# Performance work log

Measured on AMD Instinct MI355X. Metric: run time of the kernel, lower is better.

The kernel has to match this reference:

```python
import jax, jax.numpy as jnp
import numpy as np

B, C, N, D = 4, 128, 4096, 128  # batch, channels (=d_tran=out), points
BN_EPS = 1e-5


def setup_inputs() -> dict:
    key = jax.random.key(0)
    ks = jax.random.split(key, 10)
    s = 1.0 / np.sqrt(C)
    return {
        "x": jax.random.normal(ks[0], (B, C, N), dtype=jnp.float32),
        "Wqk": jax.random.uniform(ks[1], (D, C), minval=-s, maxval=s, dtype=jnp.float32),  # shared q/k weight
        "Wv": jax.random.uniform(ks[2], (D, C), minval=-s, maxval=s, dtype=jnp.float32),
        "bv": jax.random.uniform(ks[3], (D,), minval=-s, maxval=s, dtype=jnp.float32),
        "Wt": jax.random.uniform(ks[4], (C, D), minval=-s, maxval=s, dtype=jnp.float32),
        "bt": jax.random.uniform(ks[5], (C,), minval=-s, maxval=s, dtype=jnp.float32),
        "gamma": jnp.ones((C,), dtype=jnp.float32) + 0.1 * jax.random.normal(ks[6], (C,), dtype=jnp.float32),
        "beta": 0.1 * jax.random.normal(ks[7], (C,), dtype=jnp.float32),
        "rmean": 0.1 * jax.random.normal(ks[8], (C,), dtype=jnp.float32),
        "rvar": jax.random.uniform(ks[9], (C,), minval=0.5, maxval=1.5, dtype=jnp.float32),
    }


def reference(x, Wqk, Wv, bv, Wt, bt, gamma, beta, rmean, rvar):
    # x: [B, C, N]; 1x1 convs are per-point matmuls over the channel dim.
    x_q = jnp.einsum('dc,bcn->bnd', Wqk, x)                 # [B, N, D]
    x_k = jnp.einsum('dc,bcn->bdn', Wqk, x)                 # [B, D, N] (tied weight)
    x_v = jnp.einsum('dc,bcn->bdn', Wv, x) + bv[None, :, None]
    energy = jnp.einsum('bnd,bdm->bnm', x_q, x_k)           # [B, N, N]
    attention = jax.nn.softmax(energy, axis=-1)             # row softmax
    attention = attention / (1e-9 + attention.sum(axis=1, keepdims=True))  # L1 over columns
    x_r = jnp.einsum('bdn,bnm->bdm', x_v, attention)        # [B, D, N]
    y = jnp.einsum('od,bdn->bon', Wt, x - x_r) + bt[None, :, None]
    # BatchNorm1d, inference mode (running stats)
    y = gamma[None, :, None] * (y - rmean[None, :, None]) * jax.lax.rsqrt(rvar[None, :, None] + BN_EPS) + beta[None, :, None]
    return x + jax.nn.relu(y)
```

## Files before the change

kernel.cpp:

```cpp
#include <hip/hip_runtime.h>
#include <hip/hip_bf16.h>

typedef unsigned int u32;
typedef unsigned short u16;
using bf16x8 = __attribute__((ext_vector_type(8))) short;
using f32x4  = __attribute__((ext_vector_type(4))) float;
using f32x16 = __attribute__((ext_vector_type(16))) float;

#define B_ 4
#define C_ 128
#define N_ 4096
#define D_ 128
#define NS1 8
#define NSEG (N_ / NS1)
#define NCH (NSEG / 32)
#define NS2 6
#define NCHUNK (N_ / 32)

#define QS_STRIDE 136
#define VS_STRIDE 40
#define XS_STRIDE 68

__device__ __forceinline__ u16 f2bf(float f) {
    u32 x = __builtin_bit_cast(u32, f);
    x = x + 0x7fffu + ((x >> 16) & 1u);
    return (u16)(x >> 16);
}
__device__ __forceinline__ float bf2f(u16 h) {
    return __builtin_bit_cast(float, (u32)h << 16);
}
__device__ __forceinline__ u32 cvtpk(float lo, float hi) {
    u32 d;
    asm("v_cvt_pk_bf16_f32 %0, %1, %2" : "=v"(d) : "v"(lo), "v"(hi));
    return d;
}
#define EXP2 __builtin_amdgcn_exp2f
__device__ __forceinline__ bf16x8 pack8(const float* v, float s) {
    bf16x8 r;
#pragma unroll
    for (int j = 0; j < 8; ++j) r[j] = (short)f2bf(v[j] * s);
    return r;
}

__global__ __launch_bounds__(256) void k_proj(
        const float* __restrict__ x, const float* __restrict__ Wqk,
        const float* __restrict__ Wv, const float* __restrict__ bv,
        u16* __restrict__ Qbf, u16* __restrict__ Vbf) {
    __shared__ __align__(16) float xs[C_ * XS_STRIDE];
    const int bid = blockIdx.x;
    const int b  = bid >> 6;
    const int n0 = (bid & 63) << 6;
    const int t  = threadIdx.x;
    const float* xb = x + (size_t)b * C_ * N_;
#pragma unroll
    for (int i = 0; i < 8; ++i) {
        int idx = i * 256 + t;
        int c = idx >> 4, n4 = (idx & 15) * 4;
        *(float4*)&xs[c * XS_STRIDE + n4] = *(const float4*)&xb[(size_t)c * N_ + n0 + n4];
    }
    __syncthreads();
    const int lane = t & 63, w = t >> 6;
    const int l15 = lane & 15, g = lane >> 4;
    const float SC = 1.2011224087864498f;

    bf16x8 xf[4];
#pragma unroll
    for (int kk = 0; kk < 4; ++kk) {
        float tmp[8];
#pragma unroll
        for (int j = 0; j < 8; ++j) tmp[j] = xs[(kk * 32 + g * 8 + j) * XS_STRIDE + (16 * w + l15)];
        xf[kk] = pack8(tmp, 1.0f);
    }
    for (int dt = 0; dt < 8; ++dt) {
        const int d = dt * 16 + l15;
        bf16x8 wq[4], wv[4];
#pragma unroll
        for (int kk = 0; kk < 4; ++kk) {
            const float* pq = Wqk + (size_t)d * C_ + kk * 32 + g * 8;
            const float* pv = Wv  + (size_t)d * C_ + kk * 32 + g * 8;
            float a[8], c8[8];
#pragma unroll
            for (int j = 0; j < 8; ++j) { a[j] = pq[j]; c8[j] = pv[j]; }
            wq[kk] = pack8(a, SC);
            wv[kk] = pack8(c8, 1.0f);
        }
        f32x4 aq = {0.f, 0.f, 0.f, 0.f}, av = {0.f, 0.f, 0.f, 0.f};
        __builtin_amdgcn_s_setprio(1);
#pragma unroll
        for (int kk = 0; kk < 4; ++kk) {
            aq = __builtin_amdgcn_mfma_f32_16x16x32_bf16(xf[kk], wq[kk], aq, 0, 0, 0);
            av = __builtin_amdgcn_mfma_f32_16x16x32_bf16(wv[kk], xf[kk], av, 0, 0, 0);
        }
        __builtin_amdgcn_s_setprio(0);
#pragma unroll
        for (int r = 0; r < 4; ++r) {
            int nn = n0 + 16 * w + g * 4 + r;
            Qbf[((size_t)b * N_ + nn) * D_ + dt * 16 + l15] = f2bf(aq[r]);
            int dd = dt * 16 + g * 4 + r;
            Vbf[((size_t)b * D_ + dd) * N_ + n0 + 16 * w + l15] = f2bf(av[r] + bv[dd]);
        }
    }
}

__global__ __launch_bounds__(256, 4) void k_pass1(const u16* __restrict__ Qbf,
                                                  float* __restrict__ rsp) {
    __shared__ __align__(16) u16 qs[2][32 * QS_STRIDE];
    int bid = blockIdx.x;
    const int s = bid & 7; bid >>= 3;
    const int ntile = bid & 31; const int b = bid >> 5;
    const int t = threadIdx.x, lane = t & 63, w = t >> 6;
    const int l31 = lane & 31, hi = lane >> 5;
    const int nb = ntile * 128 + w * 32;

    bf16x8 bqn[8];
    {
        const u16* qn = Qbf + ((size_t)b * N_ + nb + l31) * D_ + hi * 8;
#pragma unroll
        for (int dblk = 0; dblk < 8; ++dblk) bqn[dblk] = *(const bf16x8*)(qn + dblk * 16);
    }
    const int srow = t >> 4, sslot = t & 15;
    const u16* qsrc = Qbf + ((size_t)b * N_ + s * NSEG + srow) * D_ + sslot * 8;
    const int qoff = srow * QS_STRIDE + sslot * 8;

    {
        uint4 a0 = *(const uint4*)qsrc;
        uint4 a1 = *(const uint4*)(qsrc + (size_t)16 * D_);
        *(uint4*)&qs[0][qoff] = a0;
        *(uint4*)&qs[0][qoff + 16 * QS_STRIDE] = a1;
    }
    __syncthreads();

    float rs0 = 0.f, rs1 = 0.f;
    for (int mc = 0; mc < NCH; ++mc) {
        const int cur = mc & 1;
        uint4 qpre0, qpre1;
        if (mc < NCH - 1) {
            qpre0 = *(const uint4*)(qsrc + (size_t)(mc + 1) * 32 * D_);
            qpre1 = *(const uint4*)(qsrc + (size_t)((mc + 1) * 32 + 16) * D_);
        }
        f32x16 ea, eb;
#pragma unroll
        for (int i = 0; i < 16; ++i) { ea[i] = 0.f; eb[i] = 0.f; }
        __builtin_amdgcn_s_setprio(1);
#pragma unroll
        for (int dblk = 0; dblk < 4; ++dblk) {
            bf16x8 am0 = *(const bf16x8*)(qs[cur] + l31 * QS_STRIDE + (2 * dblk + hi) * 8);
            bf16x8 am1 = *(const bf16x8*)(qs[cur] + l31 * QS_STRIDE + (2 * (dblk + 4) + hi) * 8);
            ea = __builtin_amdgcn_mfma_f32_32x32x16_bf16(am0, bqn[dblk], ea, 0, 0, 0);
            eb = __builtin_amdgcn_mfma_f32_32x32x16_bf16(am1, bqn[dblk + 4], eb, 0, 0, 0);
        }
        __builtin_amdgcn_s_setprio(0);
#pragma unroll
        for (int r = 0; r < 16; r += 2) {
            rs0 += EXP2(ea[r] + eb[r] - 64.0f);
            rs1 += EXP2(ea[r + 1] + eb[r + 1] - 64.0f);
        }
        if (mc < NCH - 1) {
            *(uint4*)&qs[cur ^ 1][qoff] = qpre0;
            *(uint4*)&qs[cur ^ 1][qoff + 16 * QS_STRIDE] = qpre1;
        }
        __syncthreads();
    }
    float rs = rs0 + rs1;
    rs += __shfl_xor(rs, 32);
    if (lane < 32) rsp[((size_t)s * B_ + b) * N_ + nb + l31] = rs;
}

__global__ void k_irs(const float* __restrict__ rsp, float* __restrict__ irs) {
    int i = blockIdx.x * 256 + threadIdx.x;
    if (i < B_ * N_) {
        float s = 0.f;
#pragma unroll
        for (int sp = 0; sp < NS1; ++sp) s += rsp[(size_t)sp * B_ * N_ + i];
        irs[i] = 1.0f / s;
    }
}

__global__ __launch_bounds__(256, 3) void k_pass2(
        const u16* __restrict__ Qbf, const u16* __restrict__ Vbf,
        const float* __restrict__ irs, u32* __restrict__ Rp32,
        float* __restrict__ csp) {
    __shared__ __align__(16) u16 qs[2][32 * QS_STRIDE];
    __shared__ __align__(16) u16 vs[2][128 * VS_STRIDE];
    int bid = blockIdx.x;
    const int s = bid % NS2; bid /= NS2;
    const int mtile = bid & 31; const int b = bid >> 5;
    const int t = threadIdx.x, lane = t & 63, w = t >> 6;
    const int l31 = lane & 31, hi = lane >> 5;
    const int m0 = mtile * 128 + w * 32;

    bf16x8 bq[8];
    {
        const u16* qm = Qbf + ((size_t)b * N_ + m0 + l31) * D_ + hi * 8;
#pragma unroll
        for (int dblk = 0; dblk < 8; ++dblk) bq[dblk] = *(const bf16x8*)(qm + dblk * 16);
    }
    f32x16 acc[4];
#pragma unroll
    for (int i = 0; i < 4; ++i)
#pragma unroll
        for (int r = 0; r < 16; ++r) acc[i][r] = 0.f;
    float cs = 0.f;
    const float* irsb = irs + (size_t)b * N_;

    const int qrow = t >> 4, qslot = t & 15;
    const u16* qsrc = Qbf + ((size_t)b * N_ + qrow) * D_ + qslot * 8;
    const int qoff = qrow * QS_STRIDE + qslot * 8;
    const int vd = t >> 2, vslot = t & 3;
    const u16* vsrc = Vbf + ((size_t)b * D_ + vd) * N_ + vslot * 8;
    const int voff = vd * VS_STRIDE + vslot * 8;

    {
        const u16* q0 = qsrc + (size_t)s * 32 * D_;
        const u16* v0 = vsrc + s * 32;
        uint4 a0 = *(const uint4*)q0;
        uint4 a1 = *(const uint4*)(q0 + (size_t)16 * D_);
        uint4 b0 = *(const uint4*)v0;
        uint4 b1 = *(const uint4*)(v0 + (size_t)64 * N_);
        *(uint4*)&qs[0][qoff] = a0;
        *(uint4*)&qs[0][qoff + 16 * QS_STRIDE] = a1;
        *(uint4*)&vs[0][voff] = b0;
        *(uint4*)&vs[0][voff + 64 * VS_STRIDE] = b1;
    }
    __syncthreads();

    int iter = 0;
    for (int c = s; c < NCHUNK; c += NS2, ++iter) {
        const int cur = iter & 1;
        const int nb = c * 32;
        const int cn = c + NS2;
        uint4 qpre0, qpre1, vpre0, vpre1;
        if (cn < NCHUNK) {
            const u16* qn = qsrc + (size_t)cn * 32 * D_;
            const u16* vn = vsrc + cn * 32;
            qpre0 = *(const uint4*)qn;
            qpre1 = *(const uint4*)(qn + (size_t)16 * D_);
            vpre0 = *(const uint4*)vn;
            vpre1 = *(const uint4*)(vn + (size_t)64 * N_);
        }
        const float* irp = irsb + nb;
        float si[32];
#pragma unroll
        for (int j = 0; j < 32; ++j) si[j] = irp[j];

        f32x16 ea, eb;
#pragma unroll
        for (int i = 0; i < 16; ++i) { ea[i] = 0.f; eb[i] = 0.f; }
        __builtin_amdgcn_s_setprio(1);
#pragma unroll
        for (int dblk = 0; dblk < 4; ++dblk) {
            bf16x8 aq0 = *(const bf16x8*)(qs[cur] + l31 * QS_STRIDE + (2 * dblk + hi) * 8);
            bf16x8 aq1 = *(const bf16x8*)(qs[cur] + l31 * QS_STRIDE + (2 * (dblk + 4) + hi) * 8);
            ea = __builtin_amdgcn_mfma_f32_32x32x16_bf16(aq0, bq[dblk], ea, 0, 0, 0);
            eb = __builtin_amdgcn_mfma_f32_32x32x16_bf16(aq1, bq[dblk + 4], eb, 0, 0, 0);
        }
        __builtin_amdgcn_s_setprio(0);
        uint4 bpA0, bpA1;
        {
            u32 A[8];
#pragma unroll
            for (int i = 0; i < 8; ++i) {
                const int cc = 2 * (i & 1) + 8 * (i >> 1);
                float ir0 = hi ? si[cc + 4] : si[cc];
                float ir1 = hi ? si[cc + 5] : si[cc + 1];
                float p0 = EXP2(ea[2 * i] + eb[2 * i] - 64.0f) * ir0;
                float p1 = EXP2(ea[2 * i + 1] + eb[2 * i + 1] - 64.0f) * ir1;
                cs += p0 + p1;
                A[i] = cvtpk(p0, p1);
            }
            u32 X0 = (u32)__shfl_xor((int)A[0], 32), X1 = (u32)__shfl_xor((int)A[1], 32);
            u32 X2 = (u32)__shfl_xor((int)A[2], 32), X3 = (u32)__shfl_xor((int)A[3], 32);
            u32 X4 = (u32)__shfl_xor((int)A[4], 32), X5 = (u32)__shfl_xor((int)A[5], 32);
            u32 X6 = (u32)__shfl_xor((int)A[6], 32), X7 = (u32)__shfl_xor((int)A[7], 32);
            bpA0 = (uint4){hi ? X2 : A[0], hi ? X3 : A[1], hi ? A[2] : X0, hi ? A[3] : X1};
            bpA1 = (uint4){hi ? X6 : A[4], hi ? X7 : A[5], hi ? A[6] : X4, hi ? A[7] : X5};
        }
        __builtin_amdgcn_s_setprio(1);
#pragma unroll
        for (int nblk = 0; nblk < 2; ++nblk) {
            bf16x8 bp = __builtin_bit_cast(bf16x8, nblk ? bpA1 : bpA0);
#pragma unroll
            for (int dblk = 0; dblk < 4; ++dblk) {
                bf16x8 av = *(const bf16x8*)(vs[cur] + (dblk * 32 + l31) * VS_STRIDE +
                                             (nblk * 2 + hi) * 8);
                acc[dblk] = __builtin_amdgcn_mfma_f32_32x32x16_bf16(av, bp, acc[dblk], 0, 0, 0);
            }
        }
        __builtin_amdgcn_s_setprio(0);
        if (cn < NCHUNK) {
            *(uint4*)&qs[cur ^ 1][qoff] = qpre0;
            *(uint4*)&qs[cur ^ 1][qoff + 16 * QS_STRIDE] = qpre1;
            *(uint4*)&vs[cur ^ 1][voff] = vpre0;
            *(uint4*)&vs[cur ^ 1][voff + 64 * VS_STRIDE] = vpre1;
        }
        __syncthreads();
    }
    cs += __shfl_xor(cs, 32);
    if (lane < 32) csp[((size_t)s * B_ + b) * N_ + m0 + l31] = cs;
    u32* rpb = Rp32 + ((size_t)s * B_ + b) * (size_t)(D_ / 2) * N_;
#pragma unroll
    for (int dblk = 0; dblk < 4; ++dblk) {
#pragma unroll
        for (int j = 0; j < 8; ++j) {
            const int row = dblk * 16 + (j & 1) + 4 * (j >> 1) + 2 * hi;
            u32 pk = cvtpk(acc[dblk][2 * j], acc[dblk][2 * j + 1]);
            rpb[(size_t)row * N_ + m0 + l31] = pk;
        }
    }
}

__global__ __launch_bounds__(512) void k_final(
        const float* __restrict__ x, const float* __restrict__ Wt,
        const float* __restrict__ bt, const float* __restrict__ gamma,
        const float* __restrict__ beta, const float* __restrict__ rmean,
        const float* __restrict__ rvar, const u32* __restrict__ Rp32,
        const float* __restrict__ csp, float* __restrict__ out) {
    __shared__ float us[128 * 65];
    __shared__ float icss[64];
    const int bid = blockIdx.x;
    const int b = bid >> 6;
    const int n0 = (bid & 63) << 6;
    const int t = threadIdx.x, lane = t & 63, w = t >> 6;
    const int l15 = lane & 15, g = lane >> 4;
    if (t < 64) {
        float s = 0.f;
#pragma unroll
        for (int sp = 0; sp < NS2; ++sp)
            s += csp[((size_t)sp * B_ + b) * N_ + n0 + t];
        icss[t] = 1.0f / (1e-9f + s);
    }
    __syncthreads();
    const float* xb = x + (size_t)b * C_ * N_;
    for (int i = 0; i < 8; ++i) {
        int idx = i * 512 + t;
        int dp = idx >> 6, n = idx & 63;
        float r0 = 0.f, r1 = 0.f;
#pragma unroll
        for (int sp = 0; sp < NS2; ++sp) {
            u32 v = Rp32[(((size_t)(sp * B_ + b) * (D_ / 2)) + dp) * N_ + n0 + n];
            r0 += bf2f((u16)(v & 0xffffu));
            r1 += bf2f((u16)(v >> 16));
        }
        float ic = icss[n];
        us[(2 * dp) * 65 + n]     = xb[(size_t)(2 * dp) * N_ + n0 + n]     - r0 * ic;
        us[(2 * dp + 1) * 65 + n] = xb[(size_t)(2 * dp + 1) * N_ + n0 + n] - r1 * ic;
    }
    __syncthreads();
    const int cg = w & 3;
    const int ct0 = (w >> 2) * 4;
    bf16x8 uf[4];
#pragma unroll
    for (int kk = 0; kk < 4; ++kk) {
        float tmp[8];
#pragma unroll
        for (int j = 0; j < 8; ++j) tmp[j] = us[(kk * 32 + g * 8 + j) * 65 + (16 * cg + l15)];
        uf[kk] = pack8(tmp, 1.0f);
    }
    for (int cti = 0; cti < 4; ++cti) {
        const int ct = ct0 + cti;
        const int c = ct * 16 + l15;
        bf16x8 wf[4];
#pragma unroll
        for (int kk = 0; kk < 4; ++kk) {
            const float* p = Wt + (size_t)c * D_ + kk * 32 + g * 8;
            float a[8];
#pragma unroll
            for (int j = 0; j < 8; ++j) a[j] = p[j];
            wf[kk] = pack8(a, 1.0f);
        }
        f32x4 acc = {0.f, 0.f, 0.f, 0.f};
        __builtin_amdgcn_s_setprio(1);
#pragma unroll
        for (int kk = 0; kk < 4; ++kk)
            acc = __builtin_amdgcn_mfma_f32_16x16x32_bf16(wf[kk], uf[kk], acc, 0, 0, 0);
        __builtin_amdgcn_s_setprio(0);
#pragma unroll
        for (int r = 0; r < 4; ++r) {
            const int cc = ct * 16 + g * 4 + r;
            const int nn = n0 + 16 * cg + l15;
            float y = acc[r] + bt[cc];
            float bn = gamma[cc] * (y - rmean[cc]) * rsqrtf(rvar[cc] + 1e-5f) + beta[cc];
            float rl = fmaxf(bn, 0.0f);
            out[((size_t)b * C_ + cc) * N_ + nn] = xb[(size_t)cc * N_ + nn] + rl;
        }
    }
}

extern "C" void kernel_launch(void* const* d_in, const int* in_sizes, int n_in,
                              void* d_out, int out_size, void* d_ws, size_t ws_size,
                              hipStream_t stream) {
    (void)in_sizes; (void)n_in; (void)out_size; (void)ws_size;
    const float* x     = (const float*)d_in[0];
    const float* Wqk   = (const float*)d_in[1];
    const float* Wv    = (const float*)d_in[2];
    const float* bv    = (const float*)d_in[3];
    const float* Wt    = (const float*)d_in[4];
    const float* bt    = (const float*)d_in[5];
    const float* gamma = (const float*)d_in[6];
    const float* beta  = (const float*)d_in[7];
    const float* rmean = (const float*)d_in[8];
    const float* rvar  = (const float*)d_in[9];
    float* out = (float*)d_out;

    char* ws = (char*)d_ws;
    u16*   Qbf = (u16*)(ws);
    u16*   Vbf = (u16*)(ws + 4194304);
    float* rsp = (float*)(ws + 8388608);
    float* irs = (float*)(ws + 8912896);
    float* csp = (float*)(ws + 8978432);
    u32*   Rp  = (u32*)(ws + 9371648);

    k_proj  <<<B_ * 64,       256, 0, stream>>>(x, Wqk, Wv, bv, Qbf, Vbf);
    k_pass1 <<<B_ * 32 * NS1, 256, 0, stream>>>(Qbf, rsp);
    k_irs   <<<(B_ * N_ + 255) / 256, 256, 0, stream>>>(rsp, irs);
    k_pass2 <<<B_ * 32 * NS2, 256, 0, stream>>>(Qbf, Vbf, irs, Rp, csp);
    k_final <<<B_ * 64,       512, 0, stream>>>(x, Wt, bt, gamma, beta, rmean, rvar, Rp, csp, out);
}
```

Baseline: 113.2 us.

## Enlarge pass1 row tile to 512 per block with 512 threads

The row-sum pass now uses 512-thread blocks. Each wave holds two 32-row Q fragments in registers, so each block covers 512 rows, and each staged key chunk in shared memory is reused across twice as many rows. To keep the grid size up, the key dimension is split into 16 segments instead of 8, which doubles the rsp partial buffer and moves the later workspace offsets. The aim is fewer global/LDS loads per MFMA, at the cost of higher register pressure and extra partial sums for k_irs to reduce.

```diff
diff --git a/kernel.cpp b/kernel.cpp
--- a/kernel.cpp
+++ b/kernel.cpp
@@ -11,7 +11,7 @@
 #define C_ 128
 #define N_ 4096
 #define D_ 128
-#define NS1 8
+#define NS1 16
 #define NSEG (N_ / NS1)
 #define NCH (NSEG / 32)
 #define NS2 6
@@ -102,21 +102,25 @@
     }
 }
 
-__global__ __launch_bounds__(256, 4) void k_pass1(const u16* __restrict__ Qbf,
+__global__ __launch_bounds__(512, 4) void k_pass1(const u16* __restrict__ Qbf,
                                                   float* __restrict__ rsp) {
     __shared__ __align__(16) u16 qs[2][32 * QS_STRIDE];
     int bid = blockIdx.x;
-    const int s = bid & 7; bid >>= 3;
-    const int ntile = bid & 31; const int b = bid >> 5;
+    const int s = bid % NS1; bid /= NS1;
+    const int ntile = bid & 7; const int b = bid >> 3;
     const int t = threadIdx.x, lane = t & 63, w = t >> 6;
     const int l31 = lane & 31, hi = lane >> 5;
-    const int nb = ntile * 128 + w * 32;
-
-    bf16x8 bqn[8];
+    const int nb0 = ntile * 512 + w * 64;
+
+    bf16x8 bqn0[8], bqn1[8];
     {
-        const u16* qn = Qbf + ((size_t)b * N_ + nb + l31) * D_ + hi * 8;
-#pragma unroll
-        for (int dblk = 0; dblk < 8; ++dblk) bqn[dblk] = *(const bf16x8*)(qn + dblk * 16);
+        const u16* qn0 = Qbf + ((size_t)b * N_ + nb0 + l31) * D_ + hi * 8;
+        const u16* qn1 = qn0 + (size_t)32 * D_;
+#pragma unroll
+        for (int dblk = 0; dblk < 8; ++dblk) {
+            bqn0[dblk] = *(const bf16x8*)(qn0 + dblk * 16);
+            bqn1[dblk] = *(const bf16x8*)(qn1 + dblk * 16);
+        }
     }
     const int srow = t >> 4, sslot = t & 15;
     const u16* qsrc = Qbf + ((size_t)b * N_ + s * NSEG + srow) * D_ + sslot * 8;
@@ -124,46 +128,63 @@
 
     {
         uint4 a0 = *(const uint4*)qsrc;
-        uint4 a1 = *(const uint4*)(qsrc + (size_t)16 * D_);
         *(uint4*)&qs[0][qoff] = a0;
-        *(uint4*)&qs[0][qoff + 16 * QS_STRIDE] = a1;
     }
     __syncthreads();
 
-    float rs0 = 0.f, rs1 = 0.f;
+    float rs0 = 0.f, rs1 = 0.f, rs2 = 0.f, rs3 = 0.f;
     for (int mc = 0; mc < NCH; ++mc) {
         const int cur = mc & 1;
-        uint4 qpre0, qpre1;
-        if (mc < NCH - 1) {
-            qpre0 = *(const uint4*)(qsrc + (size_t)(mc + 1) * 32 * D_);
-            qpre1 = *(const uint4*)(qsrc + (size_t)((mc + 1) * 32 + 16) * D_);
-        }
-        f32x16 ea, eb;
-#pragma unroll
-        for (int i = 0; i < 16; ++i) { ea[i] = 0.f; eb[i] = 0.f; }
-        __builtin_amdgcn_s_setprio(1);
-#pragma unroll
-        for (int dblk = 0; dblk < 4; ++dblk) {
-            bf16x8 am0 = *(const bf16x8*)(qs[cur] + l31 * QS_STRIDE + (2 * dblk + hi) * 8);
-            bf16x8 am1 = *(const bf16x8*)(qs[cur] + l31 * QS_STRIDE + (2 * (dblk + 4) + hi) * 8);
-            ea = __builtin_amdgcn_mfma_f32_32x32x16_bf16(am0, bqn[dblk], ea, 0, 0, 0);
-            eb = __builtin_amdgcn_mfma_f32_32x32x16_bf16(am1, bqn[dblk + 4], eb, 0, 0, 0);
-        }
-        __builtin_amdgcn_s_setprio(0);
-#pragma unroll
-        for (int r = 0; r < 16; r += 2) {
-            rs0 += EXP2(ea[r] + eb[r] - 64.0f);
-            rs1 += EXP2(ea[r + 1] + eb[r + 1] - 64.0f);
-        }
-        if (mc < NCH - 1) {
-            *(uint4*)&qs[cur ^ 1][qoff] = qpre0;
-            *(uint4*)&qs[cur ^ 1][qoff + 16 * QS_STRIDE] = qpre1;
-        }
+        uint4 qpre;
+        if (mc < NCH - 1) qpre = *(const uint4*)(qsrc + (size_t)(mc + 1) * 32 * D_);
+        {
+            f32x16 ea, eb;
+#pragma unroll
+            for (int i = 0; i < 16; ++i) { ea[i] = 0.f; eb[i] = 0.f; }
+            __builtin_amdgcn_s_setprio(1);
+#pragma unroll
+            for (int dblk = 0; dblk < 4; ++dblk) {
+                bf16x8 am0 = *(const bf16x8*)(qs[cur] + l31 * QS_STRIDE + (2 * dblk + hi) * 8);
+                bf16x8 am1 = *(const bf16x8*)(qs[cur] + l31 * QS_STRIDE + (2 * (dblk + 4) + hi) * 8);
+                ea = __builtin_amdgcn_mfma_f32_32x32x16_bf16(am0, bqn0[dblk], ea, 0, 0, 0);
+                eb = __builtin_amdgcn_mfma_f32_32x32x16_bf16(am1, bqn0[dblk + 4], eb, 0, 0, 0);
+            }
+            __builtin_amdgcn_s_setprio(0);
+#pragma unroll
+            for (int r = 0; r < 16; r += 2) {
+                rs0 += EXP2(ea[r] + eb[r] - 64.0f);
+                rs1 += EXP2(ea[r + 1] + eb[r + 1] - 64.0f);
+            }
+        }
+        {
+            f32x16 ea, eb;
+#pragma unroll
+            for (int i = 0; i < 16; ++i) { ea[i] = 0.f; eb[i] = 0.f; }
+            __builtin_amdgcn_s_setprio(1);
+#pragma unroll
+            for (int dblk = 0; dblk < 4; ++dblk) {
+                bf16x8 am0 = *(const bf16x8*)(qs[cur] + l31 * QS_STRIDE + (2 * dblk + hi) * 8);
+                bf16x8 am1 = *(const bf16x8*)(qs[cur] + l31 * QS_STRIDE + (2 * (dblk + 4) + hi) * 8);
+                ea = __builtin_amdgcn_mfma_f32_32x32x16_bf16(am0, bqn1[dblk], ea, 0, 0, 0);
+                eb = __builtin_amdgcn_mfma_f32_32x32x16_bf16(am1, bqn1[dblk + 4], eb, 0, 0, 0);
+            }
+            __builtin_amdgcn_s_setprio(0);
+#pragma unroll
+            for (int r = 0; r < 16; r += 2) {
+                rs2 += EXP2(ea[r] + eb[r] - 64.0f);
+                rs3 += EXP2(ea[r + 1] + eb[r + 1] - 64.0f);
+            }
+        }
+        if (mc < NCH - 1) *(uint4*)&qs[cur ^ 1][qoff] = qpre;
         __syncthreads();
     }
-    float rs = rs0 + rs1;
-    rs += __shfl_xor(rs, 32);
-    if (lane < 32) rsp[((size_t)s * B_ + b) * N_ + nb + l31] = rs;
+    float rsA = rs0 + rs1, rsB = rs2 + rs3;
+    rsA += __shfl_xor(rsA, 32);
+    rsB += __shfl_xor(rsB, 32);
+    if (lane < 32) {
+        rsp[((size_t)s * B_ + b) * N_ + nb0 + l31] = rsA;
+        rsp[((size_t)s * B_ + b) * N_ + nb0 + 32 + l31] = rsB;
+    }
 }
 
 __global__ void k_irs(const float* __restrict__ rsp, float* __restrict__ irs) {
@@ -406,13 +427,13 @@
     u16*   Qbf = (u16*)(ws);
     u16*   Vbf = (u16*)(ws + 4194304);
     float* rsp = (float*)(ws + 8388608);
-    float* irs = (float*)(ws + 8912896);
-    float* csp = (float*)(ws + 8978432);
-    u32*   Rp  = (u32*)(ws + 9371648);
-
-    k_proj  <<<B_ * 64,       256, 0, stream>>>(x, Wqk, Wv, bv, Qbf, Vbf);
-    k_pass1 <<<B_ * 32 * NS1, 256, 0, stream>>>(Qbf, rsp);
+    float* irs = (float*)(ws + 9437184);
+    float* csp = (float*)(ws + 9502720);
+    u32*   Rp  = (u32*)(ws + 9895936);
+
+    k_proj  <<<B_ * 64,      256, 0, stream>>>(x, Wqk, Wv, bv, Qbf, Vbf);
+    k_pass1 <<<B_ * 8 * NS1, 512, 0, stream>>>(Qbf, rsp);
     k_irs   <<<(B_ * N_ + 255) / 256, 256, 0, stream>>>(rsp, irs);
     k_pass2 <<<B_ * 32 * NS2, 256, 0, stream>>>(Qbf, Vbf, irs, Rp, csp);
-    k_final <<<B_ * 64,       512, 0, stream>>>(x, Wt, bt, gamma, beta, rmean, rvar, Rp, csp, out);
-}
+    k_final <<<B_ * 64,      512, 0, stream>>>(x, Wt, bt, gamma, beta, rmean, rvar, Rp, csp, out);
+}
```

Measured after the change: 121.8 us. +7.6%, slower.
